# Kernel optimization log

Hardware: AMD Instinct MI355X
Metric: run time of the kernel (lower is better)

## Reference

```python
import jax, jax.numpy as jnp
import numpy as np

B, DIM, H, W = 4, 384, 128, 128
HEADS = 8
EPS = 1e-12  # torch F.normalize eps


def setup_inputs() -> dict:
    key = jax.random.key(0)
    k0, k1, k2, k3 = jax.random.split(key, 4)
    x = jax.random.normal(k0, (B, DIM, H, W), jnp.float32)
    # 1x1 conv weights stored as [out, in] (kernel dims squeezed), no bias
    w_qkv = jax.random.normal(k1, (3 * DIM, DIM), jnp.float32) * 0.05
    # depthwise 3x3 conv, groups = 3*DIM -> weight [3*DIM, 1, 3, 3]
    w_dw = jax.random.normal(k2, (3 * DIM, 1, 3, 3), jnp.float32) * 0.05
    w_proj = jax.random.normal(k3, (DIM, DIM), jnp.float32) * 0.05
    temperature = jnp.ones((HEADS, 1, 1), jnp.float32)
    return {"x": x, "w_qkv": w_qkv, "w_dw": w_dw, "w_proj": w_proj,
            "temperature": temperature}


def reference(x, w_qkv, w_dw, w_proj, temperature):
    b, c, h, w = x.shape
    heads = temperature.shape[0]
    ch = c // heads  # per-head channel dim (softmax axis)

    # 1x1 conv (pointwise) == channel GEMM
    qkv = jnp.einsum('bchw,oc->bohw', x, w_qkv)  # [b, 3c, h, w]
    # depthwise 3x3 conv, padding=1
    qkv = jax.lax.conv_general_dilated(
        qkv, w_dw, window_strides=(1, 1), padding='SAME',
        feature_group_count=qkv.shape[1],
        dimension_numbers=('NCHW', 'OIHW', 'NCHW'))

    q, k, v = jnp.split(qkv, 3, axis=1)  # each [b, c, h, w]

    def to_heads(t):
        # b (head ch) h w -> b head ch (h w)
        return t.reshape(b, heads, ch, h * w)

    q, k, v = to_heads(q), to_heads(k), to_heads(v)

    # L2 normalize along spatial (last) axis, torch-style eps clamp
    q = q / jnp.maximum(jnp.linalg.norm(q, axis=-1, keepdims=True), EPS)
    k = k / jnp.maximum(jnp.linalg.norm(k, axis=-1, keepdims=True), EPS)

    # channel-wise (transposed) attention: [b, head, ch, ch]
    attn = jnp.einsum('bhcn,bhdn->bhcd', q, k) * temperature
    attn = jax.nn.softmax(attn, axis=-1)
    out = jnp.einsum('bhcd,bhdn->bhcn', attn, v)  # [b, head, ch, hw]

    out = out.reshape(b, c, h, w)
    return jnp.einsum('bchw,oc->bohw', out, w_proj)
```

## Files before the change

kernel.cpp:

```cpp
#include <hip/hip_runtime.h>
#include <math.h>

typedef unsigned short u16;
typedef unsigned int u32;
typedef __attribute__((ext_vector_type(8))) short bf16x8;
typedef __attribute__((ext_vector_type(4))) float f32x4;

#define IMG 128
#define HWN 16384
#define NTOT 65536
#define DIMC 384
#define CDIM 1152
#define NBATCH 4
#define NHEAD 8
#define CHD 48
#define KC 16

__device__ __forceinline__ u16 f2bf(float f) {
  union { float f; u32 u; } x; x.f = f;
  u32 r = x.u + 0x7fffu + ((x.u >> 16) & 1u);
  return (u16)(r >> 16);
}
__device__ __forceinline__ float bf2f(u16 v) {
  union { u32 u; float f; } x; x.u = ((u32)v) << 16;
  return x.f;
}
__device__ __forceinline__ void gload_lds16(const u16* g, u16* lds) {
  __builtin_amdgcn_global_load_lds((const __attribute__((address_space(1))) void*)g,
                                   (__attribute__((address_space(3))) void*)lds, 16, 0, 0);
}

__global__ void convert_wq_kernel(const float* __restrict__ in, u16* __restrict__ out, int n) {
  int i = blockIdx.x * 256 + threadIdx.x;
  if (i < n) out[i] = f2bf(in[i]);
}

__global__ __launch_bounds__(256) void transpose_x_kernel(const float* __restrict__ x,
                                                          u16* __restrict__ xT) {
  __shared__ float tile[32][33];
  int n0 = blockIdx.x * 32, c0 = blockIdx.y * 32, b = blockIdx.z;
  const float* xb = x + (size_t)b * DIMC * HWN;
  u16* xTb = xT + (size_t)b * HWN * DIMC;
  int tx = threadIdx.x & 31, ty = threadIdx.x >> 5;
#pragma unroll
  for (int i = 0; i < 32; i += 8)
    tile[ty + i][tx] = xb[(size_t)(c0 + ty + i) * HWN + n0 + tx];
  __syncthreads();
#pragma unroll
  for (int i = 0; i < 32; i += 8)
    xTb[(size_t)(n0 + ty + i) * DIMC + c0 + tx] = f2bf(tile[tx][ty + i]);
}

template <int BF16OUT>
__global__ __launch_bounds__(256) void gemm_bt_kernel(
    const u16* __restrict__ A, const u16* __restrict__ B, void* __restrict__ Cout,
    int MBLK, int K, int lda, int ldb, int ldc,
    unsigned long long aStride, unsigned long long bStride, unsigned long long cStride) {
  __shared__ u16 As[128 * 64];
  __shared__ u16 Bs[128 * 64];
  int bz = blockIdx.z;
  const u16* Ab = A + (size_t)bz * aStride;
  const u16* Bb = B + (size_t)bz * bStride;
  int bid = blockIdx.x;
  int xcd = bid & 7, j = bid >> 3;
  int mb = j % MBLK, nb = (j / MBLK) * 8 + xcd;
  int n0 = nb * 128, m0 = mb * 128;
  int t = threadIdx.x;
  int wave = t >> 6, lane = t & 63;
  int wm = (wave >> 1) * 64, wn = (wave & 1) * 64;
  int lr = lane & 15;
  int g4 = lane >> 4;
  int lrow = lane >> 3;
  int lswz = ((lane & 7) ^ lrow) * 8;

  f32x4 acc[4][4];
#pragma unroll
  for (int mi = 0; mi < 4; mi++)
#pragma unroll
    for (int ni = 0; ni < 4; ni++) acc[mi][ni] = (f32x4){0.f, 0.f, 0.f, 0.f};

  for (int k0 = 0; k0 < K; k0 += 64) {
#pragma unroll
    for (int i = 0; i < 4; i++) {
      int r = wave * 32 + i * 8;
      gload_lds16(Ab + (size_t)(m0 + r + lrow) * lda + k0 + lswz, &As[r * 64]);
      gload_lds16(Bb + (size_t)(n0 + r + lrow) * ldb + k0 + lswz, &Bs[r * 64]);
    }
    __syncthreads();
#pragma unroll
    for (int kk = 0; kk < 2; kk++) {
      bf16x8 af[4], bfr[4];
#pragma unroll
      for (int mi = 0; mi < 4; mi++) {
        int arow = wm + mi * 16 + lr;
        int aoct = (kk * 4 + g4) ^ (lr & 7);
        af[mi] = *(const bf16x8*)&As[arow * 64 + aoct * 8];
      }
#pragma unroll
      for (int ni = 0; ni < 4; ni++) {
        int brow = wn + ni * 16 + lr;
        int boct = (kk * 4 + g4) ^ (lr & 7);
        bfr[ni] = *(const bf16x8*)&Bs[brow * 64 + boct * 8];
      }
#pragma unroll
      for (int mi = 0; mi < 4; mi++)
#pragma unroll
        for (int ni = 0; ni < 4; ni++)
          acc[mi][ni] = __builtin_amdgcn_mfma_f32_16x16x32_bf16(af[mi], bfr[ni],
                                                                acc[mi][ni], 0, 0, 0);
    }
    __syncthreads();
  }
  int r0 = (lane >> 4) * 4;
#pragma unroll
  for (int mi = 0; mi < 4; mi++)
#pragma unroll
    for (int ni = 0; ni < 4; ni++)
#pragma unroll
      for (int r = 0; r < 4; r++) {
        int row = m0 + wm + mi * 16 + r0 + r;
        int col = n0 + wn + ni * 16 + (lane & 15);
        size_t idx = (size_t)bz * cStride + (size_t)row * ldc + col;
        if (BF16OUT)
          ((u16*)Cout)[idx] = f2bf(acc[mi][ni][r]);
        else
          ((float*)Cout)[idx] = acc[mi][ni][r];
      }
}

__global__ __launch_bounds__(256) void dwconv_planar_kernel(const u16* __restrict__ qkvP,
                                                            const float* __restrict__ w_dw,
                                                            u16* __restrict__ qkvCP,
                                                            float* __restrict__ nrmp) {
  __shared__ u16 lrows[18 * 144];
  __shared__ float red[4];
  int strip = blockIdx.x, ch = blockIdx.y, b = blockIdx.z;
  int ys = strip * 16;
  int t = threadIdx.x;
  const u16* plane = qkvP + (size_t)ch * NTOT + b * HWN;
  u16* oplane = qkvCP + (size_t)ch * NTOT + b * HWN;

#pragma unroll
  for (int it = 0; it < 2; it++) {
    int ul = t + it * 256;
    if (ul < 324) {
      int row = ul / 18, u = ul % 18;
      int gy = ys - 1 + row;
      bf16x8 v = {0, 0, 0, 0, 0, 0, 0, 0};
      if (u >= 1 && u <= 16 && gy >= 0 && gy < 128)
        v = *(const bf16x8*)&plane[gy * IMG + (u - 1) * 8];
      *(bf16x8*)((char*)lrows + row * 288 + u * 16) = v;
    }
  }
  float wt[9];
#pragma unroll
  for (int r = 0; r < 9; r++) wt[r] = w_dw[ch * 9 + r];
  __syncthreads();

  int xo = t & 15, yl = t >> 4;
  float win[3][10];
#pragma unroll
  for (int d = 0; d < 3; d++) {
    const char* base = (const char*)lrows + (yl + d) * 288 + xo * 16;
    bf16x8 rA = *(const bf16x8*)(base);
    bf16x8 rB = *(const bf16x8*)(base + 16);
    bf16x8 rC = *(const bf16x8*)(base + 32);
    win[d][0] = bf2f((u16)rA[7]);
#pragma unroll
    for (int k2 = 0; k2 < 8; k2++) win[d][k2 + 1] = bf2f((u16)rB[k2]);
    win[d][9] = bf2f((u16)rC[0]);
  }
  float accv[8] = {0.f, 0.f, 0.f, 0.f, 0.f, 0.f, 0.f, 0.f};
#pragma unroll
  for (int d = 0; d < 3; d++)
#pragma unroll
    for (int dx = 0; dx < 3; dx++) {
      float w = wt[d * 3 + dx];
#pragma unroll
      for (int jj = 0; jj < 8; jj++) accv[jj] += win[d][jj + dx] * w;
    }
  bf16x8 o;
  float n2 = 0.f;
#pragma unroll
  for (int jj = 0; jj < 8; jj++) {
    o[jj] = (short)f2bf(accv[jj]);
    n2 += accv[jj] * accv[jj];
  }
  *(bf16x8*)&oplane[(ys + yl) * IMG + xo * 8] = o;

#pragma unroll
  for (int off2 = 32; off2 >= 1; off2 >>= 1) n2 += __shfl_xor(n2, off2);
  if ((t & 63) == 0) red[t >> 6] = n2;
  __syncthreads();
  if (t == 0 && ch < 768)
    nrmp[((size_t)b * 8 + strip) * 768 + ch] = red[0] + red[1] + red[2] + red[3];
}

__global__ __launch_bounds__(256) void vtrans_kernel(const u16* __restrict__ qkvCP,
                                                     u16* __restrict__ vT) {
  __shared__ u16 tile[64][74];
  int n0 = blockIdx.x * 64, c0 = blockIdx.y * 64;
  int tx = threadIdx.x & 31, ty = threadIdx.x >> 5;
#pragma unroll
  for (int i = 0; i < 8; i++) {
    int chr = ty + i * 8;
    const u16* src = &qkvCP[(size_t)(768 + c0 + chr) * NTOT + n0 + tx * 2];
    u32 v = *(const u32*)src;
    tile[tx * 2][chr] = (u16)v;
    tile[tx * 2 + 1][chr] = (u16)(v >> 16);
  }
  __syncthreads();
#pragma unroll
  for (int i = 0; i < 8; i++) {
    int nr = ty + i * 8;
    u32 o = (u32)tile[nr][tx * 2] | ((u32)tile[nr][tx * 2 + 1] << 16);
    *(u32*)&vT[(size_t)(n0 + nr) * DIMC + c0 + tx * 2] = o;
  }
}

__global__ __launch_bounds__(256) void gram_kernel(const u16* __restrict__ qkvCP,
                                                   float* __restrict__ partials) {
  __shared__ u16 qs[48 * 136];
  __shared__ u16 ks2[48 * 136];
  __shared__ float Sred[4 * 2304];
  int kc = blockIdx.x, h = blockIdx.y, b = blockIdx.z;
  int t = threadIdx.x, wave = t >> 6, lane = t & 63;
  int lr = lane & 15, lk = (lane >> 4) * 8;
  int nbase = b * HWN + kc * (HWN / KC);

  f32x4 acc[3][3];
#pragma unroll
  for (int mi = 0; mi < 3; mi++)
#pragma unroll
    for (int ni = 0; ni < 3; ni++) acc[mi][ni] = (f32x4){0.f, 0.f, 0.f, 0.f};

  for (int tile = 0; tile < (HWN / KC) / 128; tile++) {
    int n0 = nbase + tile * 128;
    __syncthreads();
#pragma unroll
    for (int i = 0; i < 6; i++) {
      int u = t + i * 256;
      int m = (u >= 768) ? 1 : 0;
      int uu = u - m * 768;
      int r = uu >> 4, cu = uu & 15;
      int chh = m ? 384 + h * CHD + r : h * CHD + r;
      bf16x8 v = *(const bf16x8*)&qkvCP[(size_t)chh * NTOT + n0 + cu * 8];
      *(bf16x8*)((char*)(m ? ks2 : qs) + r * 272 + cu * 16) = v;
    }
    __syncthreads();
    bf16x8 af[3], bfr[3];
#pragma unroll
    for (int mi = 0; mi < 3; mi++)
      af[mi] = *(const bf16x8*)((char*)qs + (mi * 16 + lr) * 272 + wave * 64 + lk * 2);
#pragma unroll
    for (int ni = 0; ni < 3; ni++)
      bfr[ni] = *(const bf16x8*)((char*)ks2 + (ni * 16 + lr) * 272 + wave * 64 + lk * 2);
#pragma unroll
    for (int mi = 0; mi < 3; mi++)
#pragma unroll
      for (int ni = 0; ni < 3; ni++)
        acc[mi][ni] = __builtin_amdgcn_mfma_f32_16x16x32_bf16(af[mi], bfr[ni],
                                                              acc[mi][ni], 0, 0, 0);
  }

#pragma unroll
  for (int mi = 0; mi < 3; mi++)
#pragma unroll
    for (int ni = 0; ni < 3; ni++)
#pragma unroll
      for (int r = 0; r < 4; r++) {
        int crow = mi * 16 + (lane >> 4) * 4 + r;
        int dcol = ni * 16 + (lane & 15);
        Sred[wave * 2304 + crow * 48 + dcol] = acc[mi][ni][r];
      }
  __syncthreads();
  float* pout = partials + ((size_t)((b * NHEAD + h) * KC + kc)) * 2304;
  for (int idx = t; idx < 2304; idx += 256) {
    float s = 0.f;
#pragma unroll
    for (int w = 0; w < 4; w++) s += Sred[w * 2304 + idx];
    pout[idx] = s;
  }
}

__global__ __launch_bounds__(256) void softmax_kernel(const float* __restrict__ partials,
                                                      const float* __restrict__ nrmp,
                                                      const float* __restrict__ temp,
                                                      float* __restrict__ attn) {
  __shared__ float S[2304];
  __shared__ float nq[48], nk[48];
  int h = blockIdx.x, b = blockIdx.y;
  const float* p = partials + (size_t)(b * NHEAD + h) * KC * 2304;
  for (int idx = threadIdx.x; idx < 2304; idx += 256) {
    float s = 0.f;
#pragma unroll
    for (int kc = 0; kc < KC; kc++) s += p[kc * 2304 + idx];
    S[idx] = s;
  }
  if (threadIdx.x < 96) {
    int tq = threadIdx.x;
    int c = (tq < 48) ? tq : tq - 48;
    int ch = (tq < 48) ? h * CHD + c : DIMC + h * CHD + c;
    float s = 0.f;
#pragma unroll
    for (int st = 0; st < 8; st++) s += nrmp[((size_t)b * 8 + st) * 768 + ch];
    float nv = fmaxf(sqrtf(s), 1e-12f);
    if (tq < 48) nq[c] = nv; else nk[c] = nv;
  }
  __syncthreads();
  float tf = temp[h];
  float* A = attn + (size_t)(b * NHEAD + h) * 2304;
  if (threadIdx.x < CHD) {
    int c = threadIdx.x;
    float inq = 1.f / nq[c];
    float mx = -1e30f;
    float row[48];
    for (int d = 0; d < CHD; d++) {
      float v = S[c * 48 + d] * tf * inq / nk[d];
      row[d] = v;
      mx = fmaxf(mx, v);
    }
    float sum = 0.f;
    for (int d = 0; d < CHD; d++) {
      float e = expf(row[d] - mx);
      row[d] = e;
      sum += e;
    }
    float inv = 1.f / sum;
    for (int d = 0; d < CHD; d++) A[c * 48 + d] = row[d] * inv;
  }
}

__global__ __launch_bounds__(256) void build_mf_kernel(const float* __restrict__ attn,
                                                       const float* __restrict__ w_proj,
                                                       u16* __restrict__ Mf) {
  __shared__ float al[NHEAD * 2304];
  int b = blockIdx.y, o0 = blockIdx.x * 32;
  for (int i = threadIdx.x; i < NHEAD * 2304; i += 256)
    al[i] = attn[(size_t)b * NHEAD * 2304 + i];
  __syncthreads();
  for (int idx = threadIdx.x; idx < 32 * DIMC; idx += 256) {
    int ol = idx / DIMC, cp = idx % DIMC;
    int o = o0 + ol, h = cp / CHD, d = cp % CHD;
    float s = 0.f;
#pragma unroll
    for (int c = 0; c < CHD; c++)
      s += w_proj[(size_t)o * DIMC + h * CHD + c] * al[h * 2304 + c * 48 + d];
    Mf[((size_t)b * DIMC + o) * DIMC + cp] = f2bf(s);
  }
}

extern "C" void kernel_launch(void* const* d_in, const int* in_sizes, int n_in,
                              void* d_out, int out_size, void* d_ws, size_t ws_size,
                              hipStream_t stream) {
  const float* x      = (const float*)d_in[0];
  const float* w_qkv  = (const float*)d_in[1];
  const float* w_dw   = (const float*)d_in[2];
  const float* w_proj = (const float*)d_in[3];
  const float* temp   = (const float*)d_in[4];
  float* out = (float*)d_out;

  char* ws = (char*)d_ws;
  size_t off = 0;
  u16* xT = (u16*)(ws + off);
  size_t xT_off = off;
  off += (size_t)NTOT * DIMC * 2;
  u16* qkvP = (u16*)(ws + off);
  off += (size_t)CDIM * NTOT * 2;
  u16* qkvCP = (u16*)(ws + off);
  off += (size_t)CDIM * NTOT * 2;
  u16* wq16 = (u16*)(ws + off);
  off += (size_t)CDIM * DIMC * 2;
  float* nrmp = (float*)(ws + off);
  off += (size_t)NBATCH * 8 * 768 * 4;
  float* partials = (float*)(ws + off);
  off += (size_t)NBATCH * NHEAD * KC * 2304 * 4;
  float* attn = (float*)(ws + off);
  off += (size_t)NBATCH * NHEAD * 2304 * 4;
  u16* Mf = (u16*)(ws + off);
  off += (size_t)NBATCH * DIMC * DIMC * 2;
  u16* vT = (u16*)(ws + xT_off);

  if (ws_size < off) return;

  convert_wq_kernel<<<dim3((CDIM * DIMC + 255) / 256), dim3(256), 0, stream>>>(
      w_qkv, wq16, CDIM * DIMC);
  transpose_x_kernel<<<dim3(HWN / 32, DIMC / 32, NBATCH), dim3(256), 0, stream>>>(x, xT);
  gemm_bt_kernel<1><<<dim3(4608, 1, 1), dim3(256), 0, stream>>>(
      wq16, xT, (void*)qkvP, 9, DIMC, DIMC, DIMC, NTOT, 0ULL, 0ULL, 0ULL);
  dwconv_planar_kernel<<<dim3(8, CDIM, NBATCH), dim3(256), 0, stream>>>(
      qkvP, w_dw, qkvCP, nrmp);
  vtrans_kernel<<<dim3(NTOT / 64, DIMC / 64), dim3(256), 0, stream>>>(qkvCP, vT);
  gram_kernel<<<dim3(KC, NHEAD, NBATCH), dim3(256), 0, stream>>>(qkvCP, partials);
  softmax_kernel<<<dim3(NHEAD, NBATCH), dim3(256), 0, stream>>>(partials, nrmp, temp, attn);
  build_mf_kernel<<<dim3(DIMC / 32, NBATCH), dim3(256), 0, stream>>>(attn, w_proj, Mf);
  gemm_bt_kernel<0><<<dim3(384, 1, NBATCH), dim3(256), 0, stream>>>(
      Mf, vT, (void*)out, 3, DIMC, DIMC, DIMC, HWN,
      (unsigned long long)DIMC * DIMC, (unsigned long long)HWN * DIMC,
      (unsigned long long)DIMC * HWN);
}
```

Measured before the change: 355.2 us.

## Fuse V-channel depthwise conv with transpose into a single kernel

The depthwise 3x3 conv now runs only over the q/k channels in the planar kernel. A new kernel computes the conv for the v channels and writes the result directly in the transposed [n, c] layout through a shared-memory tile. This drops the intermediate planar v buffer write and its re-read by the separate transpose kernel, and shrinks the workspace. The fused kernel reloads three input rows per output row, which adds some redundant reads of qkvP.

```diff
diff --git a/kernel.cpp b/kernel.cpp
--- a/kernel.cpp
+++ b/kernel.cpp
@@ -192,29 +192,79 @@
   for (int off2 = 32; off2 >= 1; off2 >>= 1) n2 += __shfl_xor(n2, off2);
   if ((t & 63) == 0) red[t >> 6] = n2;
   __syncthreads();
-  if (t == 0 && ch < 768)
+  if (t == 0)
     nrmp[((size_t)b * 8 + strip) * 768 + ch] = red[0] + red[1] + red[2] + red[3];
 }
 
-__global__ __launch_bounds__(256) void vtrans_kernel(const u16* __restrict__ qkvCP,
-                                                     u16* __restrict__ vT) {
-  __shared__ u16 tile[64][74];
-  int n0 = blockIdx.x * 64, c0 = blockIdx.y * 64;
-  int tx = threadIdx.x & 31, ty = threadIdx.x >> 5;
-#pragma unroll
-  for (int i = 0; i < 8; i++) {
-    int chr = ty + i * 8;
-    const u16* src = &qkvCP[(size_t)(768 + c0 + chr) * NTOT + n0 + tx * 2];
-    u32 v = *(const u32*)src;
-    tile[tx * 2][chr] = (u16)v;
-    tile[tx * 2 + 1][chr] = (u16)(v >> 16);
-  }
-  __syncthreads();
-#pragma unroll
-  for (int i = 0; i < 8; i++) {
-    int nr = ty + i * 8;
-    u32 o = (u32)tile[nr][tx * 2] | ((u32)tile[nr][tx * 2 + 1] << 16);
-    *(u32*)&vT[(size_t)(n0 + nr) * DIMC + c0 + tx * 2] = o;
+__global__ __launch_bounds__(256) void dwconv_vtrans_kernel(const u16* __restrict__ qkvP,
+                                                            const float* __restrict__ w_dw,
+                                                            u16* __restrict__ vT) {
+  __shared__ u16 in3[3 * 64 * 144];
+  __shared__ u16 ot[128 * 72];
+  int y = blockIdx.x, cg = blockIdx.y, b = blockIdx.z;
+  int t = threadIdx.x;
+  int ch0 = 768 + cg * 64;
+
+#pragma unroll
+  for (int it = 0; it < 2; it++) {
+    int ul = t + it * 256;
+    if (ul < 384) {
+      int d = ul >> 7, r = ul & 127;
+      int ch = r >> 1, side = r & 1;
+      *(bf16x8*)&in3[(d * 64 + ch) * 144 + side * 136] = (bf16x8){0, 0, 0, 0, 0, 0, 0, 0};
+    }
+  }
+#pragma unroll
+  for (int i = 0; i < 12; i++) {
+    int u = t + i * 256;
+    int d = u >> 10, ch = (u >> 4) & 63, o = u & 15;
+    int yn = y - 1 + d;
+    bf16x8 v = {0, 0, 0, 0, 0, 0, 0, 0};
+    if (yn >= 0 && yn < 128)
+      v = *(const bf16x8*)&qkvP[(size_t)(ch0 + ch) * NTOT + b * HWN + yn * IMG + o * 8];
+    *(bf16x8*)&in3[(d * 64 + ch) * 144 + 8 + o * 8] = v;
+  }
+  int c = t & 63;
+  float wt[9];
+#pragma unroll
+  for (int r = 0; r < 9; r++) wt[r] = w_dw[(ch0 + c) * 9 + r];
+  __syncthreads();
+
+#pragma unroll
+  for (int i = 0; i < 4; i++) {
+    int oct = (t >> 6) + i * 4;
+    float win[3][10];
+#pragma unroll
+    for (int d = 0; d < 3; d++) {
+      const u16* base = &in3[(d * 64 + c) * 144 + oct * 8];
+      bf16x8 rA = *(const bf16x8*)(base);
+      bf16x8 rB = *(const bf16x8*)(base + 8);
+      bf16x8 rC = *(const bf16x8*)(base + 16);
+      win[d][0] = bf2f((u16)rA[7]);
+#pragma unroll
+      for (int k2 = 0; k2 < 8; k2++) win[d][k2 + 1] = bf2f((u16)rB[k2]);
+      win[d][9] = bf2f((u16)rC[0]);
+    }
+    float accv[8] = {0.f, 0.f, 0.f, 0.f, 0.f, 0.f, 0.f, 0.f};
+#pragma unroll
+    for (int d = 0; d < 3; d++)
+#pragma unroll
+      for (int dx = 0; dx < 3; dx++) {
+        float w = wt[d * 3 + dx];
+#pragma unroll
+        for (int jj = 0; jj < 8; jj++) accv[jj] += win[d][jj + dx] * w;
+      }
+#pragma unroll
+    for (int jj = 0; jj < 8; jj++) ot[(oct * 8 + jj) * 72 + c] = f2bf(accv[jj]);
+  }
+  __syncthreads();
+
+#pragma unroll
+  for (int i = 0; i < 4; i++) {
+    int u = t + i * 256;
+    int px = u >> 3, co = u & 7;
+    bf16x8 v = *(const bf16x8*)&ot[px * 72 + co * 8];
+    *(bf16x8*)&vT[((size_t)b * HWN + y * IMG + px) * DIMC + cg * 64 + co * 8] = v;
   }
 }
 
@@ -368,7 +418,7 @@
   u16* qkvP = (u16*)(ws + off);
   off += (size_t)CDIM * NTOT * 2;
   u16* qkvCP = (u16*)(ws + off);
-  off += (size_t)CDIM * NTOT * 2;
+  off += (size_t)768 * NTOT * 2;
   u16* wq16 = (u16*)(ws + off);
   off += (size_t)CDIM * DIMC * 2;
   float* nrmp = (float*)(ws + off);
@@ -388,9 +438,9 @@
   transpose_x_kernel<<<dim3(HWN / 32, DIMC / 32, NBATCH), dim3(256), 0, stream>>>(x, xT);
   gemm_bt_kernel<1><<<dim3(4608, 1, 1), dim3(256), 0, stream>>>(
       wq16, xT, (void*)qkvP, 9, DIMC, DIMC, DIMC, NTOT, 0ULL, 0ULL, 0ULL);
-  dwconv_planar_kernel<<<dim3(8, CDIM, NBATCH), dim3(256), 0, stream>>>(
+  dwconv_planar_kernel<<<dim3(8, 768, NBATCH), dim3(256), 0, stream>>>(
       qkvP, w_dw, qkvCP, nrmp);
-  vtrans_kernel<<<dim3(NTOT / 64, DIMC / 64), dim3(256), 0, stream>>>(qkvCP, vT);
+  dwconv_vtrans_kernel<<<dim3(IMG, 6, NBATCH), dim3(256), 0, stream>>>(qkvP, w_dw, vT);
   gram_kernel<<<dim3(KC, NHEAD, NBATCH), dim3(256), 0, stream>>>(qkvCP, partials);
   softmax_kernel<<<dim3(NHEAD, NBATCH), dim3(256), 0, stream>>>(partials, nrmp, temp, attn);
   build_mf_kernel<<<dim3(DIMC / 32, NBATCH), dim3(256), 0, stream>>>(attn, w_proj, Mf);
```

Result: no change. 356.5 us (+0.4%).
